# Kernel optimization log

Hardware: AMD Instinct MI355X
Metric: run time of the kernel (lower is better)

Reference implementation:

```python
import jax, jax.numpy as jnp
import numpy as np

NF = 256  # node_feat_size
GF = 256  # graph_feat_size
V = 262144
G = 4096


def setup_inputs() -> dict:
    key = jax.random.key(0)
    ks = jax.random.split(key, 12)
    node_feats = jax.random.normal(ks[0], (V, NF), dtype=jnp.float32)
    g_feats = jax.random.normal(ks[1], (G, GF), dtype=jnp.float32)
    segment_ids = jnp.sort(jax.random.randint(ks[2], (V,), 0, G, dtype=jnp.int32))
    s = 0.05
    # compute_logits: Linear(NF+GF -> 1)
    Wl = jax.random.normal(ks[3], (1, NF + GF), dtype=jnp.float32) * s
    bl = jnp.zeros((1,), dtype=jnp.float32)
    # project_nodes: Linear(NF -> GF)  (dropout=0 -> identity)
    Wp = jax.random.normal(ks[4], (GF, NF), dtype=jnp.float32) * s
    bp = jnp.zeros((GF,), dtype=jnp.float32)
    # GRUCell(GF, GF), torch gate order (r, z, n)
    W_ih = jax.random.normal(ks[5], (3 * GF, GF), dtype=jnp.float32) * s
    W_hh = jax.random.normal(ks[6], (3 * GF, GF), dtype=jnp.float32) * s
    b_ih = jnp.zeros((3 * GF,), dtype=jnp.float32)
    b_hh = jnp.zeros((3 * GF,), dtype=jnp.float32)
    return dict(node_feats=node_feats, g_feats=g_feats, segment_ids=segment_ids,
                Wl=Wl, bl=bl, Wp=Wp, bp=bp,
                W_ih=W_ih, W_hh=W_hh, b_ih=b_ih, b_hh=b_hh)


def reference(node_feats, g_feats, segment_ids, Wl, bl, Wp, bp, W_ih, W_hh, b_ih, b_hh):
    num_graphs = g_feats.shape[0]
    # broadcast relu(g_feats) to nodes, concat with node feats, logits Linear + LeakyReLU
    gb = jax.nn.relu(g_feats)[segment_ids]                      # [V, GF]
    cat = jnp.concatenate([gb, node_feats], axis=1)             # [V, GF+NF]
    z = jax.nn.leaky_relu(cat @ Wl.T + bl, negative_slope=0.01) # [V, 1]
    # segmented softmax over nodes per graph
    m = jax.ops.segment_max(z, segment_ids, num_segments=num_graphs,
                            indices_are_sorted=True)            # [G, 1]
    e = jnp.exp(z - m[segment_ids])                             # [V, 1]
    denom = jax.ops.segment_sum(e, segment_ids, num_segments=num_graphs,
                                indices_are_sorted=True)        # [G, 1]
    a = e / denom[segment_ids]                                  # [V, 1]
    # project nodes (dropout p=0 -> identity) and weighted sum per graph
    hv = node_feats @ Wp.T + bp                                 # [V, GF]
    context = jax.ops.segment_sum(a * hv, segment_ids, num_segments=num_graphs,
                                  indices_are_sorted=True)      # [G, GF]
    context = jax.nn.elu(context)
    # GRUCell: input=context, hidden=g_feats, torch gate order r,z,n
    gi = context @ W_ih.T + b_ih                                # [G, 3*GF]
    gh = g_feats @ W_hh.T + b_hh                                # [G, 3*GF]
    i_r, i_z, i_n = jnp.split(gi, 3, axis=1)
    h_r, h_z, h_n = jnp.split(gh, 3, axis=1)
    r = jax.nn.sigmoid(i_r + h_r)
    u = jax.nn.sigmoid(i_z + h_z)
    n = jnp.tanh(i_n + r * h_n)
    h_new = (1.0 - u) * n + u * g_feats
    return h_new
```

## Files before the change

kernel.cpp:

```cpp
#include <hip/hip_runtime.h>
#include <hip/hip_bf16.h>
#include <stdint.h>

typedef unsigned short u16;
typedef __attribute__((ext_vector_type(8))) short short8;
typedef __attribute__((ext_vector_type(4))) float floatx4;

#define NFEAT 256

__device__ __forceinline__ unsigned short f2b(float f) {
    unsigned int x = __builtin_bit_cast(unsigned int, f);
    x += 0x7fffu + ((x >> 16) & 1u);
    return (unsigned short)(x >> 16);
}
__device__ __forceinline__ float sigmoidf_(float x) {
    return 1.0f / (1.0f + __expf(-x));
}

__global__ void __launch_bounds__(256)
k0_prep(const int* __restrict__ seg, int V, int G, int* __restrict__ off,
        const float* __restrict__ Wp, const float* __restrict__ Wih,
        const float* __restrict__ Whh,
        u16* __restrict__ wpb, u16* __restrict__ wihb, u16* __restrict__ whhb)
{
    const int i = blockIdx.x * 256 + threadIdx.x;

    {
        const int n1 = 256 * 256;
        const int n2 = n1 + 768 * 256;
        const int n3 = n2 + 768 * 256;
        int idx = i * 2;
        if (idx < n3) {
            const float* src; u16* dst; int o;
            if (idx < n1)      { src = Wp;  dst = wpb;  o = idx; }
            else if (idx < n2) { src = Wih; dst = wihb; o = idx - n1; }
            else               { src = Whh; dst = whhb; o = idx - n2; }
            float2 v = *(const float2*)(src + o);
            dst[o]     = f2b(v.x);
            dst[o + 1] = f2b(v.y);
        }
    }

    if (i < V) {
        int s = seg[i];
        int prev = (i == 0) ? -1 : seg[i - 1];
        if (s != prev) {
            for (int g2 = prev + 1; g2 <= s; ++g2) off[g2] = i;
        }
        if (i == V - 1) {
            for (int g2 = s + 1; g2 <= G; ++g2) off[g2] = V;
        }
    }
}

__global__ void __launch_bounds__(256)
k1_attn_pool(const float* __restrict__ nf, const float* __restrict__ gf,
             const int* __restrict__ off, const float* __restrict__ Wl,
             const float* __restrict__ bl,
             u16* __restrict__ s_out,
             float* __restrict__ pres, u16* __restrict__ gfb)
{
    const int g = blockIdx.x;
    const int t = threadIdx.x;
    const int lane = t & 63;
    const int wv = t >> 6;
    __shared__ float red[4];
    __shared__ float accs[4][256];
    __shared__ float lws[4];

    const int start = off[g];
    const int count = off[g + 1] - start;

    const float* base = nf + (size_t)start * NFEAT + lane * 4;
    float4 x[4] = {{0,0,0,0},{0,0,0,0},{0,0,0,0},{0,0,0,0}};
    #pragma unroll
    for (int r = 0; r < 4; ++r) {
        int i = wv * 4 + r;
        if (i < count) x[r] = *(const float4*)(base + (size_t)i * NFEAT);
    }

    const float4 wn = *(const float4*)(Wl + NFEAT + lane * 4);

    const float gfv = gf[(size_t)g * NFEAT + t];
    gfb[(size_t)g * NFEAT + t] = f2b(gfv);
    float v = fmaxf(gfv, 0.0f) * Wl[t];
    #pragma unroll
    for (int o = 32; o > 0; o >>= 1) v += __shfl_xor(v, o);
    if (lane == 0) red[wv] = v;
    __syncthreads();
    const float gbase = (red[0] + red[1]) + (red[2] + red[3]) + bl[0];

    float l = 0.0f;
    float4 acc = {0.f, 0.f, 0.f, 0.f};
    for (int i = wv * 4; i < count; i += 16) {
        float4 nx[4] = {{0,0,0,0},{0,0,0,0},{0,0,0,0},{0,0,0,0}};
        #pragma unroll
        for (int r = 0; r < 4; ++r) {
            if (i + 16 + r < count) nx[r] = *(const float4*)(base + (size_t)(i + 16 + r) * NFEAT);
        }
        float d[4];
        #pragma unroll
        for (int r = 0; r < 4; ++r)
            d[r] = x[r].x * wn.x + x[r].y * wn.y + x[r].z * wn.z + x[r].w * wn.w;
        #pragma unroll
        for (int o = 32; o > 0; o >>= 1) {
            #pragma unroll
            for (int r = 0; r < 4; ++r) d[r] += __shfl_xor(d[r], o);
        }
        #pragma unroll
        for (int r = 0; r < 4; ++r) {
            float z = d[r] + gbase;
            z = (z > 0.0f) ? z : 0.01f * z;
            float p = (i + r < count) ? __expf(z) : 0.0f;
            l += p;
            acc.x += p * x[r].x;
            acc.y += p * x[r].y;
            acc.z += p * x[r].z;
            acc.w += p * x[r].w;
        }
        x[0] = nx[0]; x[1] = nx[1]; x[2] = nx[2]; x[3] = nx[3];
    }

    accs[wv][lane * 4 + 0] = acc.x;
    accs[wv][lane * 4 + 1] = acc.y;
    accs[wv][lane * 4 + 2] = acc.z;
    accs[wv][lane * 4 + 3] = acc.w;
    if (lane == 0) lws[wv] = l;
    __syncthreads();

    const float L = (lws[0] + lws[1]) + (lws[2] + lws[3]);
    const float sv = (accs[0][t] + accs[1][t]) + (accs[2][t] + accs[3][t]);
    const float inv = (L > 0.0f) ? 1.0f / L : 0.0f;
    s_out[(size_t)g * NFEAT + t] = f2b(sv * inv);
    if (t == 0) pres[g] = (count > 0) ? 1.0f : 0.0f;
}

#define CTX_LD 264
__global__ void __launch_bounds__(512)
k2_fused(const u16* __restrict__ s, const u16* __restrict__ wpb,
         const float* __restrict__ bp, const float* __restrict__ pres,
         const u16* __restrict__ gfb, const float* __restrict__ gf,
         const u16* __restrict__ wihb, const u16* __restrict__ whhb,
         const float* __restrict__ bih, const float* __restrict__ bhh,
         float* __restrict__ out)
{
    __shared__ u16 ctx[16][CTX_LD];
    const int t = threadIdx.x;
    const int w = t >> 6;
    const int lane = t & 63;
    const int m0 = blockIdx.x * 16;
    const int lr = lane & 15;
    const int kh = lane >> 4;

    {
        const short* A = (const short*)s + (size_t)(m0 + lr) * NFEAT + kh * 8;
        short8 af[8];
        #pragma unroll
        for (int kk = 0; kk < 8; ++kk) af[kk] = *(const short8*)(A + kk * 32);

        #pragma unroll
        for (int nt = 0; nt < 2; ++nt) {
            const int n0 = (w * 2 + nt) * 16;
            const short* B = (const short*)wpb + (size_t)(n0 + lr) * NFEAT + kh * 8;
            floatx4 acc = {0.f, 0.f, 0.f, 0.f};
            #pragma unroll
            for (int kk = 0; kk < 8; ++kk)
                acc = __builtin_amdgcn_mfma_f32_16x16x32_bf16(af[kk], *(const short8*)(B + kk * 32), acc, 0, 0, 0);
            const int col = n0 + lr;
            const float bias = bp[col];
            #pragma unroll
            for (int r = 0; r < 4; ++r) {
                int rl = kh * 4 + r;
                float x = acc[r] + bias * pres[m0 + rl];
                x = (x > 0.0f) ? x : (__expf(x) - 1.0f);
                ctx[rl][col] = f2b(x);
            }
        }
    }
    __syncthreads();

    short8 a1[8], a2[8];
    #pragma unroll
    for (int kk = 0; kk < 8; ++kk)
        a1[kk] = *(const short8*)&ctx[lr][kk * 32 + kh * 8];
    {
        const short* A2 = (const short*)gfb + (size_t)(m0 + lr) * NFEAT + kh * 8;
        #pragma unroll
        for (int kk = 0; kk < 8; ++kk) a2[kk] = *(const short8*)(A2 + kk * 32);
    }

    #pragma unroll
    for (int jt = 0; jt < 2; ++jt) {
        const int j0 = (w * 2 + jt) * 16;
        const size_t boff = (size_t)(j0 + lr) * NFEAT + kh * 8;
        const short* Bir = (const short*)wihb + boff;
        const short* Biz = Bir + 256 * NFEAT;
        const short* Bin = Bir + 512 * NFEAT;
        const short* Bhr = (const short*)whhb + boff;
        const short* Bhz = Bhr + 256 * NFEAT;
        const short* Bhn = Bhr + 512 * NFEAT;

        floatx4 air = {0,0,0,0}, aiz = {0,0,0,0}, ain = {0,0,0,0};
        floatx4 ahr = {0,0,0,0}, ahz = {0,0,0,0}, ahn = {0,0,0,0};
        #pragma unroll
        for (int kk = 0; kk < 8; ++kk) {
            const int k = kk * 32;
            air = __builtin_amdgcn_mfma_f32_16x16x32_bf16(a1[kk], *(const short8*)(Bir + k), air, 0, 0, 0);
            aiz = __builtin_amdgcn_mfma_f32_16x16x32_bf16(a1[kk], *(const short8*)(Biz + k), aiz, 0, 0, 0);
            ain = __builtin_amdgcn_mfma_f32_16x16x32_bf16(a1[kk], *(const short8*)(Bin + k), ain, 0, 0, 0);
            ahr = __builtin_amdgcn_mfma_f32_16x16x32_bf16(a2[kk], *(const short8*)(Bhr + k), ahr, 0, 0, 0);
            ahz = __builtin_amdgcn_mfma_f32_16x16x32_bf16(a2[kk], *(const short8*)(Bhz + k), ahz, 0, 0, 0);
            ahn = __builtin_amdgcn_mfma_f32_16x16x32_bf16(a2[kk], *(const short8*)(Bhn + k), ahn, 0, 0, 0);
        }
        const int col = j0 + lr;
        const float b_ir = bih[col], b_iz = bih[256 + col], b_in = bih[512 + col];
        const float b_hr = bhh[col], b_hz = bhh[256 + col], b_hn = bhh[512 + col];
        #pragma unroll
        for (int r = 0; r < 4; ++r) {
            int row = m0 + kh * 4 + r;
            float rg = sigmoidf_((air[r] + b_ir) + (ahr[r] + b_hr));
            float ug = sigmoidf_((aiz[r] + b_iz) + (ahz[r] + b_hz));
            float ng = tanhf((ain[r] + b_in) + rg * (ahn[r] + b_hn));
            float h  = gf[(size_t)row * NFEAT + col];
            out[(size_t)row * NFEAT + col] = (1.0f - ug) * ng + ug * h;
        }
    }
}

extern "C" void kernel_launch(void* const* d_in, const int* in_sizes, int n_in,
                              void* d_out, int out_size, void* d_ws, size_t ws_size,
                              hipStream_t stream)
{
    const float* nf  = (const float*)d_in[0];
    const float* gf  = (const float*)d_in[1];
    const int*   seg = (const int*)d_in[2];
    const float* Wl  = (const float*)d_in[3];
    const float* bl  = (const float*)d_in[4];
    const float* Wp  = (const float*)d_in[5];
    const float* bp  = (const float*)d_in[6];
    const float* Wih = (const float*)d_in[7];
    const float* Whh = (const float*)d_in[8];
    const float* bih = (const float*)d_in[9];
    const float* bhh = (const float*)d_in[10];

    const int V = in_sizes[2];
    const int G = in_sizes[1] / NFEAT;

    char* ws = (char*)d_ws;
    u16*   sbuf = (u16*)ws;                           ws += (size_t)G * NFEAT * 2;
    u16*   gfb  = (u16*)ws;                           ws += (size_t)G * NFEAT * 2;
    u16*   wpb  = (u16*)ws;                           ws += (size_t)256 * 256 * 2;
    u16*   wihb = (u16*)ws;                           ws += (size_t)768 * 256 * 2;
    u16*   whhb = (u16*)ws;                           ws += (size_t)768 * 256 * 2;
    float* pres = (float*)ws;                         ws += (size_t)G * 4;
    int*   off  = (int*)ws;                           ws += (size_t)(G + 1) * 4;

    k0_prep<<<(V + 255) / 256, 256, 0, stream>>>(seg, V, G, off, Wp, Wih, Whh,
                                                 wpb, wihb, whhb);
    k1_attn_pool<<<G, 256, 0, stream>>>(nf, gf, off, Wl, bl, sbuf, pres, gfb);
    k2_fused<<<G / 16, 512, 0, stream>>>(sbuf, wpb, bp, pres, gfb, gf,
                                         wihb, whhb, bih, bhh, (float*)d_out);
    (void)ws_size; (void)n_in; (void)out_size;
}
```

Measured before the change: 420.4 us.

## Split node pooling into fixed node chunks with atomic segment accumulation

Result: no change. 422.9 us (+0.6%).

```diff
diff --git a/kernel.cpp b/kernel.cpp
--- a/kernel.cpp
+++ b/kernel.cpp
@@ -18,18 +18,25 @@
 }
 
 __global__ void __launch_bounds__(256)
-k0_prep(const int* __restrict__ seg, int V, int G, int* __restrict__ off,
+k0_prep(const float* __restrict__ gf, const float* __restrict__ Wl,
+        const float* __restrict__ bl,
         const float* __restrict__ Wp, const float* __restrict__ Wih,
         const float* __restrict__ Whh,
-        u16* __restrict__ wpb, u16* __restrict__ wihb, u16* __restrict__ whhb)
-{
-    const int i = blockIdx.x * 256 + threadIdx.x;
+        u16* __restrict__ gfb, float* __restrict__ gbase,
+        u16* __restrict__ wpb, u16* __restrict__ wihb, u16* __restrict__ whhb,
+        float* __restrict__ sacc, float* __restrict__ lacc, int G)
+{
+    const int blk = blockIdx.x;
+    const int t = threadIdx.x;
+    const int lane = t & 63;
+    const int w = t >> 6;
+    const int gid = blk * 256 + t;
 
     {
         const int n1 = 256 * 256;
         const int n2 = n1 + 768 * 256;
         const int n3 = n2 + 768 * 256;
-        int idx = i * 2;
+        int idx = gid * 2;
         if (idx < n3) {
             const float* src; u16* dst; int o;
             if (idx < n1)      { src = Wp;  dst = wpb;  o = idx; }
@@ -41,63 +48,61 @@
         }
     }
 
-    if (i < V) {
-        int s = seg[i];
-        int prev = (i == 0) ? -1 : seg[i - 1];
-        if (s != prev) {
-            for (int g2 = prev + 1; g2 <= s; ++g2) off[g2] = i;
-        }
-        if (i == V - 1) {
-            for (int g2 = s + 1; g2 <= G; ++g2) off[g2] = V;
-        }
+    {
+        const int g = blk * 4 + w;
+        if (g < G) {
+            float4 gv = *(const float4*)(gf + (size_t)g * NFEAT + lane * 4);
+            ushort4 b4 = { f2b(gv.x), f2b(gv.y), f2b(gv.z), f2b(gv.w) };
+            *(ushort4*)(gfb + (size_t)g * NFEAT + lane * 4) = b4;
+            float4 wv = *(const float4*)(Wl + lane * 4);
+            float v = fmaxf(gv.x, 0.f) * wv.x + fmaxf(gv.y, 0.f) * wv.y
+                    + fmaxf(gv.z, 0.f) * wv.z + fmaxf(gv.w, 0.f) * wv.w;
+            #pragma unroll
+            for (int o = 32; o > 0; o >>= 1) v += __shfl_xor(v, o);
+            if (lane == 0) gbase[g] = v + bl[0];
+        }
+    }
+
+    {
+        float4 z4 = {0.f, 0.f, 0.f, 0.f};
+        size_t idx4 = (size_t)gid * 4;
+        if (idx4 < (size_t)G * NFEAT) *(float4*)(sacc + idx4) = z4;
+        if (gid < G) lacc[gid] = 0.0f;
     }
 }
 
 __global__ void __launch_bounds__(256)
-k1_attn_pool(const float* __restrict__ nf, const float* __restrict__ gf,
-             const int* __restrict__ off, const float* __restrict__ Wl,
-             const float* __restrict__ bl,
-             u16* __restrict__ s_out,
-             float* __restrict__ pres, u16* __restrict__ gfb)
-{
-    const int g = blockIdx.x;
+k1_attn_pool(const float* __restrict__ nf, const int* __restrict__ seg,
+             const float* __restrict__ Wl, const float* __restrict__ gbase,
+             float* __restrict__ sacc, float* __restrict__ lacc, int V)
+{
     const int t = threadIdx.x;
     const int lane = t & 63;
-    const int wv = t >> 6;
-    __shared__ float red[4];
-    __shared__ float accs[4][256];
-    __shared__ float lws[4];
-
-    const int start = off[g];
-    const int count = off[g + 1] - start;
-
-    const float* base = nf + (size_t)start * NFEAT + lane * 4;
-    float4 x[4] = {{0,0,0,0},{0,0,0,0},{0,0,0,0},{0,0,0,0}};
+    const int w = t >> 6;
+    const int s0 = blockIdx.x * 512 + w * 128;
+    const int end = s0 + 128;
+
+    const float4 wn = *(const float4*)(Wl + NFEAT + lane * 4);
+    const float* base = nf + (size_t)s0 * NFEAT + lane * 4;
+
+    float4 x[4];
     #pragma unroll
-    for (int r = 0; r < 4; ++r) {
-        int i = wv * 4 + r;
-        if (i < count) x[r] = *(const float4*)(base + (size_t)i * NFEAT);
-    }
-
-    const float4 wn = *(const float4*)(Wl + NFEAT + lane * 4);
-
-    const float gfv = gf[(size_t)g * NFEAT + t];
-    gfb[(size_t)g * NFEAT + t] = f2b(gfv);
-    float v = fmaxf(gfv, 0.0f) * Wl[t];
-    #pragma unroll
-    for (int o = 32; o > 0; o >>= 1) v += __shfl_xor(v, o);
-    if (lane == 0) red[wv] = v;
-    __syncthreads();
-    const float gbase = (red[0] + red[1]) + (red[2] + red[3]) + bl[0];
-
+    for (int r = 0; r < 4; ++r) x[r] = *(const float4*)(base + (size_t)r * NFEAT);
+
+    int gcur = seg[s0];
+    float gb = gbase[gcur];
+    float4 acc = {0.f, 0.f, 0.f, 0.f};
     float l = 0.0f;
-    float4 acc = {0.f, 0.f, 0.f, 0.f};
-    for (int i = wv * 4; i < count; i += 16) {
+
+    for (int i = s0; i < end; i += 4) {
         float4 nx[4] = {{0,0,0,0},{0,0,0,0},{0,0,0,0},{0,0,0,0}};
-        #pragma unroll
-        for (int r = 0; r < 4; ++r) {
-            if (i + 16 + r < count) nx[r] = *(const float4*)(base + (size_t)(i + 16 + r) * NFEAT);
-        }
+        if (i + 4 < end) {
+            #pragma unroll
+            for (int r = 0; r < 4; ++r)
+                nx[r] = *(const float4*)(base + (size_t)(i + 4 + r - s0) * NFEAT);
+        }
+        const int4 sg = *(const int4*)(seg + i);
+
         float d[4];
         #pragma unroll
         for (int r = 0; r < 4; ++r)
@@ -107,11 +112,27 @@
             #pragma unroll
             for (int r = 0; r < 4; ++r) d[r] += __shfl_xor(d[r], o);
         }
+
+        const int sgr[4] = { sg.x, sg.y, sg.z, sg.w };
         #pragma unroll
         for (int r = 0; r < 4; ++r) {
-            float z = d[r] + gbase;
+            if (sgr[r] != gcur) {
+                if (l > 0.0f) {
+                    float* dst = sacc + (size_t)gcur * NFEAT + lane * 4;
+                    atomicAdd(dst + 0, acc.x);
+                    atomicAdd(dst + 1, acc.y);
+                    atomicAdd(dst + 2, acc.z);
+                    atomicAdd(dst + 3, acc.w);
+                    if (lane == 0) atomicAdd(lacc + gcur, l);
+                }
+                gcur = sgr[r];
+                gb = gbase[gcur];
+                acc.x = acc.y = acc.z = acc.w = 0.f;
+                l = 0.f;
+            }
+            float z = d[r] + gb;
             z = (z > 0.0f) ? z : 0.01f * z;
-            float p = (i + r < count) ? __expf(z) : 0.0f;
+            float p = __expf(z);
             l += p;
             acc.x += p * x[r].x;
             acc.y += p * x[r].y;
@@ -120,25 +141,21 @@
         }
         x[0] = nx[0]; x[1] = nx[1]; x[2] = nx[2]; x[3] = nx[3];
     }
-
-    accs[wv][lane * 4 + 0] = acc.x;
-    accs[wv][lane * 4 + 1] = acc.y;
-    accs[wv][lane * 4 + 2] = acc.z;
-    accs[wv][lane * 4 + 3] = acc.w;
-    if (lane == 0) lws[wv] = l;
-    __syncthreads();
-
-    const float L = (lws[0] + lws[1]) + (lws[2] + lws[3]);
-    const float sv = (accs[0][t] + accs[1][t]) + (accs[2][t] + accs[3][t]);
-    const float inv = (L > 0.0f) ? 1.0f / L : 0.0f;
-    s_out[(size_t)g * NFEAT + t] = f2b(sv * inv);
-    if (t == 0) pres[g] = (count > 0) ? 1.0f : 0.0f;
+    if (l > 0.0f) {
+        float* dst = sacc + (size_t)gcur * NFEAT + lane * 4;
+        atomicAdd(dst + 0, acc.x);
+        atomicAdd(dst + 1, acc.y);
+        atomicAdd(dst + 2, acc.z);
+        atomicAdd(dst + 3, acc.w);
+        if (lane == 0) atomicAdd(lacc + gcur, l);
+    }
 }
 
 #define CTX_LD 264
 __global__ void __launch_bounds__(512)
-k2_fused(const u16* __restrict__ s, const u16* __restrict__ wpb,
-         const float* __restrict__ bp, const float* __restrict__ pres,
+k2_fused(const float* __restrict__ sacc, const float* __restrict__ lacc,
+         const u16* __restrict__ wpb,
+         const float* __restrict__ bp,
          const u16* __restrict__ gfb, const float* __restrict__ gf,
          const u16* __restrict__ wihb, const u16* __restrict__ whhb,
          const float* __restrict__ bih, const float* __restrict__ bhh,
@@ -153,10 +170,21 @@
     const int kh = lane >> 4;
 
     {
-        const short* A = (const short*)s + (size_t)(m0 + lr) * NFEAT + kh * 8;
+        const float* A = sacc + (size_t)(m0 + lr) * NFEAT + kh * 8;
+        const float lrow = lacc[m0 + lr];
+        const float inv = (lrow > 0.0f) ? 1.0f / lrow : 0.0f;
         short8 af[8];
         #pragma unroll
-        for (int kk = 0; kk < 8; ++kk) af[kk] = *(const short8*)(A + kk * 32);
+        for (int kk = 0; kk < 8; ++kk) {
+            float4 a0 = *(const float4*)(A + kk * 32);
+            float4 a1 = *(const float4*)(A + kk * 32 + 4);
+            short8 v;
+            v[0] = (short)f2b(a0.x * inv); v[1] = (short)f2b(a0.y * inv);
+            v[2] = (short)f2b(a0.z * inv); v[3] = (short)f2b(a0.w * inv);
+            v[4] = (short)f2b(a1.x * inv); v[5] = (short)f2b(a1.y * inv);
+            v[6] = (short)f2b(a1.z * inv); v[7] = (short)f2b(a1.w * inv);
+            af[kk] = v;
+        }
 
         #pragma unroll
         for (int nt = 0; nt < 2; ++nt) {
@@ -171,7 +199,8 @@
             #pragma unroll
             for (int r = 0; r < 4; ++r) {
                 int rl = kh * 4 + r;
-                float x = acc[r] + bias * pres[m0 + rl];
+                float presv = (lacc[m0 + rl] > 0.0f) ? 1.0f : 0.0f;
+                float x = acc[r] + bias * presv;
                 x = (x > 0.0f) ? x : (__expf(x) - 1.0f);
                 ctx[rl][col] = f2b(x);
             }
@@ -247,18 +276,20 @@
     const int G = in_sizes[1] / NFEAT;
 
     char* ws = (char*)d_ws;
-    u16*   sbuf = (u16*)ws;                           ws += (size_t)G * NFEAT * 2;
+    float* sacc = (float*)ws;                         ws += (size_t)G * NFEAT * 4;
+    float* lacc = (float*)ws;                         ws += (size_t)G * 4;
+    float* gbase= (float*)ws;                         ws += (size_t)G * 4;
     u16*   gfb  = (u16*)ws;                           ws += (size_t)G * NFEAT * 2;
     u16*   wpb  = (u16*)ws;                           ws += (size_t)256 * 256 * 2;
     u16*   wihb = (u16*)ws;                           ws += (size_t)768 * 256 * 2;
     u16*   whhb = (u16*)ws;                           ws += (size_t)768 * 256 * 2;
-    float* pres = (float*)ws;                         ws += (size_t)G * 4;
-    int*   off  = (int*)ws;                           ws += (size_t)(G + 1) * 4;
-
-    k0_prep<<<(V + 255) / 256, 256, 0, stream>>>(seg, V, G, off, Wp, Wih, Whh,
-                                                 wpb, wihb, whhb);
-    k1_attn_pool<<<G, 256, 0, stream>>>(nf, gf, off, Wl, bl, sbuf, pres, gfb);
-    k2_fused<<<G / 16, 512, 0, stream>>>(sbuf, wpb, bp, pres, gfb, gf,
+
+    const int k0_blocks = (G * NFEAT / 4 + 255) / 256;
+    k0_prep<<<k0_blocks, 256, 0, stream>>>(gf, Wl, bl, Wp, Wih, Whh,
+                                           gfb, gbase, wpb, wihb, whhb,
+                                           sacc, lacc, G);
+    k1_attn_pool<<<V / 512, 256, 0, stream>>>(nf, seg, Wl, gbase, sacc, lacc, V);
+    k2_fused<<<G / 16, 512, 0, stream>>>(sacc, lacc, wpb, bp, gfb, gf,
                                          wihb, whhb, bih, bhh, (float*)d_out);
     (void)ws_size; (void)n_in; (void)out_size;
 }
```
